# Kernel optimization log

Hardware: AMD Instinct MI355X
Metric: run time of the kernel (lower is better)

Reference implementation:

```python
import jax, jax.numpy as jnp
import numpy as np

K = 3
PAD = 1
KP = K * K


def setup_inputs() -> dict:
    key = jax.random.key(0)
    k1, k2, k3, k4 = jax.random.split(key, 4)
    B, C, O, H, W = 8, 64, 64, 128, 128
    x = jax.random.normal(k1, (B, C, H, W), dtype=jnp.float32)
    offset = jax.random.normal(k2, (B, 2 * KP, H, W), dtype=jnp.float32)
    weight = jax.random.normal(k3, (O, C, K, K), dtype=jnp.float32) * 0.05
    bias = jax.random.normal(k4, (O,), dtype=jnp.float32) * 0.05
    return {"x": x, "offset": offset, "weight": weight, "bias": bias}


def _deform_conv(x, offset, weight, bias):
    B, C, H, W = x.shape
    O = weight.shape[0]
    x_pad = jnp.pad(x, ((0, 0), (0, 0), (PAD, PAD), (PAD, PAD)))
    Hp, Wp = H + 2 * PAD, W + 2 * PAD
    dt = x.dtype

    # kernel-point grid, row-major (yy, xx) as in torch meshgrid 'ij'
    r = K // 2
    rng = jnp.arange(-r, r + 1, dtype=dt)
    ky = jnp.repeat(rng, K)          # [KP]
    kx = jnp.tile(rng, K)            # [KP]

    base_y = jnp.arange(H, dtype=dt) + PAD
    base_x = jnp.arange(W, dtype=dt) + PAD

    off = offset.reshape(B, KP, 2, H, W)
    # sample coords in padded-image space; grid_sample align_corners=True
    # normalization cancels exactly, so sample at (cy, cx) directly.
    cy = base_y[None, None, :, None] + ky[None, :, None, None] + off[:, :, 0]  # [B,KP,H,W]
    cx = base_x[None, None, None, :] + kx[None, :, None, None] + off[:, :, 1]

    y0 = jnp.floor(cy)
    x0 = jnp.floor(cx)
    wy1 = cy - y0
    wx1 = cx - x0
    wy0 = 1.0 - wy1
    wx0 = 1.0 - wx1

    flat = x_pad.reshape(B, C, Hp * Wp)

    def gather(yi, xi):
        # zeros padding: out-of-bounds corner pixels contribute 0
        valid = ((yi >= 0) & (yi <= Hp - 1) & (xi >= 0) & (xi <= Wp - 1)).astype(dt)
        yc = jnp.clip(yi, 0, Hp - 1).astype(jnp.int32)
        xc = jnp.clip(xi, 0, Wp - 1).astype(jnp.int32)
        idx = (yc * Wp + xc).reshape(B, 1, KP * H * W)
        g = jnp.take_along_axis(flat, jnp.broadcast_to(idx, (B, C, KP * H * W)), axis=2)
        g = g.reshape(B, C, KP, H, W)
        return g * valid[:, None]  # broadcast valid [B,1,KP,H,W]

    sampled = (wy0 * wx0)[:, None] * gather(y0, x0) \
            + (wy0 * wx1)[:, None] * gather(y0, x0 + 1) \
            + (wy1 * wx0)[:, None] * gather(y0 + 1, x0) \
            + (wy1 * wx1)[:, None] * gather(y0 + 1, x0 + 1)  # [B,C,KP,H,W]

    w3 = weight.reshape(O, C, KP)
    out = jnp.einsum('bcphw,ocp->bohw', sampled, w3) + bias[None, :, None, None]
    return out


def reference(x, offset, weight, bias):
    return _deform_conv(x, offset, weight, bias)
```

## Files before the change

### kernel.cpp

```cpp
#include <hip/hip_runtime.h>
#include <hip/hip_bf16.h>

#define BB 8
#define CC 64
#define OO 64
#define HH 128
#define WW 128
#define HP 130
#define WP 130
#define KP 9

typedef __attribute__((ext_vector_type(8))) _Float16 f16x8;
typedef __attribute__((ext_vector_type(2))) _Float16 h2;
typedef __attribute__((ext_vector_type(4))) float f32x4;
typedef __attribute__((ext_vector_type(4))) unsigned u32x4;

#define ROWB 16640u

static __device__ __forceinline__ unsigned short f2h(float f) {
  _Float16 h = (_Float16)f;
  return __builtin_bit_cast(unsigned short, h);
}
static __device__ __forceinline__ h2 asH2(unsigned u) {
  return __builtin_bit_cast(h2, u);
}
static __device__ __forceinline__ unsigned asU32(h2 v) {
  return __builtin_bit_cast(unsigned, v);
}

__global__ __launch_bounds__(256) void k_xpose(const float* __restrict__ x,
                                               unsigned short* __restrict__ xt) {
  __shared__ unsigned short tile[128][66];
  int wg0 = blockIdx.x;
  int wg = (wg0 & 7) * 128 + (wg0 >> 3);
  int h = wg & 127, b = wg >> 7;
  int t = threadIdx.x;
  int w = t & 127, chalf = t >> 7;
  const float* xp = x + ((size_t)(b * CC) * HH + h) * WW;
#pragma unroll 4
  for (int c2 = 0; c2 < 32; ++c2) {
    int c = c2 * 2 + chalf;
    float v = xp[(size_t)c * HH * WW + w];
    tile[w][c] = f2h(v);
  }
  __syncthreads();
  int c = t & 63, w2 = t >> 6;
  unsigned short* xtb = xt + (size_t)b * HP * WP * CC;
#pragma unroll 4
  for (int w4 = 0; w4 < 32; ++w4) {
    int ww = w4 * 4 + w2;
    xtb[((size_t)(h + 1) * WP + (ww + 1)) * CC + c] = tile[ww][c];
  }
  if (t < 128) {
    int xx = (t >= 64) ? (WP - 1) : 0;
    xtb[((size_t)(h + 1) * WP + xx) * CC + (t & 63)] = 0;
  }
  if (h == 0) {
    for (int i = t; i < 2 * WP * CC; i += 256) {
      int top = (i < WP * CC);
      int rem = top ? i : i - WP * CC;
      size_t y = top ? 0 : (HP - 1);
      xtb[y * WP * CC + rem] = 0;
    }
  }
}

__global__ __launch_bounds__(256) void k_wfrag(const float* __restrict__ wsrc,
                                               unsigned short* __restrict__ wf) {
  int flat = blockIdx.x * 256 + threadIdx.x;
  int j = flat & 7;
  int lane = (flat >> 3) & 63;
  int nf = (flat >> 9) & 3;
  int ks = (flat >> 11) & 1;
  int p = flat >> 12;
  int c = ks * 32 + ((lane >> 4) * 8) + j;
  int o = nf * 16 + (lane & 15);
  wf[flat] = f2h(wsrc[(size_t)(o * CC + c) * KP + p]);
}

__global__ __launch_bounds__(256) void k_deform_main(const float* __restrict__ offset,
                                                     const float* __restrict__ bias,
                                                     const unsigned short* __restrict__ xt,
                                                     const unsigned short* __restrict__ wf,
                                                     float* __restrict__ out) {
  __shared__ __align__(16) char lds[20992];
  int wg0 = blockIdx.x;
  int wgs = (wg0 & 7) * 256 + (wg0 >> 3);
  int tile = wgs & 1, h = (wgs >> 1) & 127, b = wgs >> 8;
  int w0 = tile * 64;
  int t = threadIdx.x, wave = t >> 6, lane = t & 63;

  char* S0 = lds;
  uint2* cw = reinterpret_cast<uint2*>(lds + 16384) + wave * 144;

#pragma unroll
  for (int it = 0; it < 3; ++it) {
    int pair = it * 64 + lane;
    if (pair < 144) {
      int p = pair >> 4, pxl = pair & 15;
      int px = wave * 16 + pxl;
      int w = w0 + px;
      const float* offp = offset + (((size_t)b * 18 + 2 * p) * HH + h) * WW + w;
      float offy = offp[0];
      float offx = offp[HH * WW];
      float cy = (float)(h + p / 3) + offy;
      float cx = (float)(w + p % 3) + offx;
      float y0f = floorf(cy), x0f = floorf(cx);
      float wy1 = cy - y0f, wx1 = cx - x0f;
      int iy0 = (int)y0f, ix0 = (int)x0f;
      int iy0c = min(max(iy0, 0), HP - 1);
      int iy1c = min(max(iy0 + 1, 0), HP - 1);
      int ix0c = min(max(ix0, 0), WP - 1);
      int ix1c = min(max(ix0 + 1, 0), WP - 1);
      unsigned w0p = (unsigned)((iy0c * WP + ix0c) * (CC * 2));
      if (ix1c != ix0c) w0p |= (1u << 30);
      if (iy1c != iy0c) w0p |= (1u << 31);
      unsigned hv;
      asm("v_cvt_pkrtz_f16_f32 %0, %1, %2" : "=v"(hv) : "v"(wy1), "v"(wx1));
      uint2 ce;
      ce.x = w0p;
      ce.y = hv;
      cw[pair] = ce;
    }
  }

  f32x4 acc[4];
#pragma unroll
  for (int m = 0; m < 4; ++m) acc[m] = (f32x4){0.f, 0.f, 0.f, 0.f};

  const char* xb = (const char*)(xt + (size_t)b * HP * WP * CC);
  int c8 = lane & 7, pg = lane >> 3;
  unsigned cb = (unsigned)c8 * 16;
  unsigned swz = cb ^ ((unsigned)pg << 4);
  const uint2* cwl = cw + pg;

#define GLOADX(dst, voff) \
  asm volatile("global_load_dwordx4 %0, %1, %2" \
               : "=v"(dst) : "v"(voff), "s"(xb) : "memory")
#define GLOADW(dst, voff) \
  asm volatile("global_load_dwordx4 %0, %1, %2" \
               : "=v"(dst) : "v"(voff), "s"(wf) : "memory")

  auto LOADC = [&](int p, uint2* eo) {
#pragma unroll
    for (int it = 0; it < 2; ++it) eo[it] = cwl[p * 16 + it * 8];
  };
  auto ISSUE = [&](const uint2* ei, u32x4* go) {
#pragma unroll
    for (int it = 0; it < 2; ++it) {
      unsigned w0p = ei[it].x;
      unsigned a00 = (w0p & 0x003FFFFFu) + cb;
      unsigned dx = ((w0p >> 30) & 1u) << 7;
      unsigned dy = (w0p & 0x80000000u) ? ROWB : 0u;
      unsigned a01 = a00 + dx, a10 = a00 + dy, a11 = a10 + dx;
      GLOADX(go[it * 4 + 0], a00);
      GLOADX(go[it * 4 + 1], a01);
      GLOADX(go[it * 4 + 2], a10);
      GLOADX(go[it * 4 + 3], a11);
    }
  };
  auto BUILD = [&](const uint2* ei, const u32x4* gi, char* Sc) {
    char* swave = Sc + wave * 2048 + pg * 128;
#pragma unroll
    for (int it = 0; it < 2; ++it) {
      h2 wyx = asH2(ei[it].y);
      _Float16 wy = wyx.x, wx = wyx.y;
      _Float16 w11 = wy * wx;
      _Float16 w01 = wx - w11;
      _Float16 w10 = wy - w11;
      _Float16 w00 = (_Float16)1.0f - wx - w10;
      h2 W00 = {w00, w00}, W01 = {w01, w01}, W10 = {w10, w10}, W11 = {w11, w11};
      u32x4 q00 = gi[it * 4 + 0], q01 = gi[it * 4 + 1];
      u32x4 q10 = gi[it * 4 + 2], q11 = gi[it * 4 + 3];
      u32x4 pk;
#pragma unroll
      for (int k = 0; k < 4; ++k) {
        h2 s = W00 * asH2(q00[k]) + W01 * asH2(q01[k])
             + W10 * asH2(q10[k]) + W11 * asH2(q11[k]);
        pk[k] = asU32(s);
      }
      *reinterpret_cast<u32x4*>(swave + it * 1024 + swz) = pk;
    }
  };
  auto MFMA = [&](const char* Sc, f16x8 b0, f16x8 b1) {
    int l15 = lane & 15, kc = (lane >> 4) * 16, sw = (lane & 7) << 4;
#pragma unroll
    for (int m = 0; m < 4; ++m) {
      int rb = (m * 16 + l15) * 128;
      f16x8 a0 = *reinterpret_cast<const f16x8*>(Sc + rb + (kc ^ sw));
      f16x8 a1 = *reinterpret_cast<const f16x8*>(Sc + rb + ((64 + kc) ^ sw));
      acc[m] = __builtin_amdgcn_mfma_f32_16x16x32_f16(a0, b0, acc[m], 0, 0, 0);
      acc[m] = __builtin_amdgcn_mfma_f32_16x16x32_f16(a1, b1, acc[m], 0, 0, 0);
    }
  };

  uint2 e[2];
  u32x4 g[8];
  LOADC(0, e);
  ISSUE(e, g);
#pragma unroll
  for (int p = 0; p < 9; ++p) {
    char* Sc = S0 + (p & 1) * 8192;
    f16x8 bv0, bv1;
    unsigned wfo = (unsigned)((p * 8 + wave) * 1024 + lane * 16);
    GLOADW(bv0, wfo);
    GLOADW(bv1, wfo + 4096);
    asm volatile("s_waitcnt vmcnt(2)" ::: "memory");
    __builtin_amdgcn_sched_barrier(0);
    BUILD(e, g, Sc);
    if (p < 8) LOADC(p + 1, e);
    asm volatile("s_waitcnt lgkmcnt(0)" ::: "memory");
    __builtin_amdgcn_s_barrier();
    if (p < 8) {
      ISSUE(e, g);
      asm volatile("s_waitcnt vmcnt(8)" ::: "memory");
    } else {
      asm volatile("s_waitcnt vmcnt(0)" ::: "memory");
    }
    __builtin_amdgcn_sched_barrier(0);
    MFMA(Sc, bv0, bv1);
  }
#undef GLOADX
#undef GLOADW

  __syncthreads();
  float* S2 = reinterpret_cast<float*>(lds);
  int l15 = lane & 15;
#pragma unroll
  for (int m = 0; m < 4; ++m) {
#pragma unroll
    for (int i2 = 0; i2 < 4; ++i2) {
      int px = m * 16 + ((lane >> 4) * 4) + i2;
      int o = wave * 16 + l15;
      S2[px * 65 + o] = acc[m][i2];
    }
  }
  __syncthreads();
  {
    int px = t & 63, o2 = t >> 6;
    float* op = out + (((size_t)b * OO) * HH + h) * WW + w0 + px;
#pragma unroll
    for (int o4 = 0; o4 < 16; ++o4) {
      int o = o4 * 4 + o2;
      op[(size_t)o * HH * WW] = S2[px * 65 + o] + bias[o];
    }
  }
}

extern "C" void kernel_launch(void* const* d_in, const int* in_sizes, int n_in,
                              void* d_out, int out_size, void* d_ws, size_t ws_size,
                              hipStream_t stream) {
  const float* x = (const float*)d_in[0];
  const float* offset = (const float*)d_in[1];
  const float* weight = (const float*)d_in[2];
  const float* bias = (const float*)d_in[3];
  float* out = (float*)d_out;

  unsigned short* xt = (unsigned short*)d_ws;
  unsigned short* wf = (unsigned short*)((char*)d_ws + 17305600);

  k_xpose<<<BB * HH, 256, 0, stream>>>(x, xt);
  k_wfrag<<<144, 256, 0, stream>>>(weight, wf);
  k_deform_main<<<BB * HH * 2, 256, 0, stream>>>(offset, bias, xt, wf, out);
}
```

Measured before the change: 48.52 us.

## Fold weight repack into transpose kernel and retile main kernel to 32-pixel blocks

The separate weight-fragment kernel is merged into the transpose kernel: its first 144 blocks also write the fp16 weight fragments, which removes one kernel launch. The main deform kernel now uses 2 waves of 128 threads covering 32 pixels per block instead of 4 waves covering 64 pixels. Each wave now computes 32 output channels using two MFMA N-fragments, and the grid is doubled. The aim is a smaller LDS footprint and more resident blocks for better latency hiding. In exchange, each wave loads more weight registers, and there are twice as many blocks, each paying its own setup and epilogue cost.

```diff
diff --git a/kernel.cpp b/kernel.cpp
--- a/kernel.cpp
+++ b/kernel.cpp
@@ -29,12 +29,25 @@
 }
 
 __global__ __launch_bounds__(256) void k_xpose(const float* __restrict__ x,
-                                               unsigned short* __restrict__ xt) {
+                                               const float* __restrict__ wsrc,
+                                               unsigned short* __restrict__ xt,
+                                               unsigned short* __restrict__ wf) {
   __shared__ unsigned short tile[128][66];
   int wg0 = blockIdx.x;
+  int t = threadIdx.x;
+  if (wg0 < 144) {
+    int flat = wg0 * 256 + t;
+    int j = flat & 7;
+    int lane = (flat >> 3) & 63;
+    int nf = (flat >> 9) & 3;
+    int ks = (flat >> 11) & 1;
+    int p = flat >> 12;
+    int c = ks * 32 + ((lane >> 4) * 8) + j;
+    int o = nf * 16 + (lane & 15);
+    wf[flat] = f2h(wsrc[(size_t)(o * CC + c) * KP + p]);
+  }
   int wg = (wg0 & 7) * 128 + (wg0 >> 3);
   int h = wg & 127, b = wg >> 7;
-  int t = threadIdx.x;
   int w = t & 127, chalf = t >> 7;
   const float* xp = x + ((size_t)(b * CC) * HH + h) * WW;
 #pragma unroll 4
@@ -65,41 +78,27 @@
   }
 }
 
-__global__ __launch_bounds__(256) void k_wfrag(const float* __restrict__ wsrc,
-                                               unsigned short* __restrict__ wf) {
-  int flat = blockIdx.x * 256 + threadIdx.x;
-  int j = flat & 7;
-  int lane = (flat >> 3) & 63;
-  int nf = (flat >> 9) & 3;
-  int ks = (flat >> 11) & 1;
-  int p = flat >> 12;
-  int c = ks * 32 + ((lane >> 4) * 8) + j;
-  int o = nf * 16 + (lane & 15);
-  wf[flat] = f2h(wsrc[(size_t)(o * CC + c) * KP + p]);
-}
-
-__global__ __launch_bounds__(256) void k_deform_main(const float* __restrict__ offset,
+__global__ __launch_bounds__(128) void k_deform_main(const float* __restrict__ offset,
                                                      const float* __restrict__ bias,
                                                      const unsigned short* __restrict__ xt,
                                                      const unsigned short* __restrict__ wf,
                                                      float* __restrict__ out) {
-  __shared__ __align__(16) char lds[20992];
+  __shared__ __align__(16) char lds[10496];
   int wg0 = blockIdx.x;
-  int wgs = (wg0 & 7) * 256 + (wg0 >> 3);
-  int tile = wgs & 1, h = (wgs >> 1) & 127, b = wgs >> 8;
-  int w0 = tile * 64;
+  int wgs = (wg0 & 7) * 512 + (wg0 >> 3);
+  int tile = wgs & 3, h = (wgs >> 2) & 127, b = wgs >> 9;
+  int w0 = tile * 32;
   int t = threadIdx.x, wave = t >> 6, lane = t & 63;
 
   char* S0 = lds;
-  uint2* cw = reinterpret_cast<uint2*>(lds + 16384) + wave * 144;
+  uint2* cw = reinterpret_cast<uint2*>(lds + 8192) + wave * 144;
 
 #pragma unroll
   for (int it = 0; it < 3; ++it) {
     int pair = it * 64 + lane;
     if (pair < 144) {
       int p = pair >> 4, pxl = pair & 15;
-      int px = wave * 16 + pxl;
-      int w = w0 + px;
+      int w = w0 + wave * 16 + pxl;
       const float* offp = offset + (((size_t)b * 18 + 2 * p) * HH + h) * WW + w;
       float offy = offp[0];
       float offx = offp[HH * WW];
@@ -182,15 +181,17 @@
       *reinterpret_cast<u32x4*>(swave + it * 1024 + swz) = pk;
     }
   };
-  auto MFMA = [&](const char* Sc, f16x8 b0, f16x8 b1) {
+  auto MFMA = [&](const char* Sc, f16x8 b00, f16x8 b01, f16x8 b10, f16x8 b11) {
     int l15 = lane & 15, kc = (lane >> 4) * 16, sw = (lane & 7) << 4;
 #pragma unroll
-    for (int m = 0; m < 4; ++m) {
+    for (int m = 0; m < 2; ++m) {
       int rb = (m * 16 + l15) * 128;
       f16x8 a0 = *reinterpret_cast<const f16x8*>(Sc + rb + (kc ^ sw));
       f16x8 a1 = *reinterpret_cast<const f16x8*>(Sc + rb + ((64 + kc) ^ sw));
-      acc[m] = __builtin_amdgcn_mfma_f32_16x16x32_f16(a0, b0, acc[m], 0, 0, 0);
-      acc[m] = __builtin_amdgcn_mfma_f32_16x16x32_f16(a1, b1, acc[m], 0, 0, 0);
+      acc[m * 2 + 0] = __builtin_amdgcn_mfma_f32_16x16x32_f16(a0, b00, acc[m * 2 + 0], 0, 0, 0);
+      acc[m * 2 + 0] = __builtin_amdgcn_mfma_f32_16x16x32_f16(a1, b01, acc[m * 2 + 0], 0, 0, 0);
+      acc[m * 2 + 1] = __builtin_amdgcn_mfma_f32_16x16x32_f16(a0, b10, acc[m * 2 + 1], 0, 0, 0);
+      acc[m * 2 + 1] = __builtin_amdgcn_mfma_f32_16x16x32_f16(a1, b11, acc[m * 2 + 1], 0, 0, 0);
     }
   };
 
@@ -200,12 +201,14 @@
   ISSUE(e, g);
 #pragma unroll
   for (int p = 0; p < 9; ++p) {
-    char* Sc = S0 + (p & 1) * 8192;
-    f16x8 bv0, bv1;
-    unsigned wfo = (unsigned)((p * 8 + wave) * 1024 + lane * 16);
-    GLOADW(bv0, wfo);
-    GLOADW(bv1, wfo + 4096);
-    asm volatile("s_waitcnt vmcnt(2)" ::: "memory");
+    char* Sc = S0 + (p & 1) * 4096;
+    f16x8 bv00, bv01, bv10, bv11;
+    unsigned wfo = (unsigned)((p * 8 + wave * 2) * 1024 + lane * 16);
+    GLOADW(bv00, wfo);
+    GLOADW(bv01, wfo + 4096);
+    GLOADW(bv10, wfo + 1024);
+    GLOADW(bv11, wfo + 5120);
+    asm volatile("s_waitcnt vmcnt(4)" ::: "memory");
     __builtin_amdgcn_sched_barrier(0);
     BUILD(e, g, Sc);
     if (p < 8) LOADC(p + 1, e);
@@ -218,7 +221,7 @@
       asm volatile("s_waitcnt vmcnt(0)" ::: "memory");
     }
     __builtin_amdgcn_sched_barrier(0);
-    MFMA(Sc, bv0, bv1);
+    MFMA(Sc, bv00, bv01, bv10, bv11);
   }
 #undef GLOADX
 #undef GLOADW
@@ -227,17 +230,20 @@
   float* S2 = reinterpret_cast<float*>(lds);
   int l15 = lane & 15;
 #pragma unroll
-  for (int m = 0; m < 4; ++m) {
-#pragma unroll
-    for (int i2 = 0; i2 < 4; ++i2) {
-      int px = m * 16 + ((lane >> 4) * 4) + i2;
-      int o = wave * 16 + l15;
-      S2[px * 65 + o] = acc[m][i2];
+  for (int m = 0; m < 2; ++m) {
+#pragma unroll
+    for (int nf = 0; nf < 2; ++nf) {
+#pragma unroll
+      for (int i2 = 0; i2 < 4; ++i2) {
+        int px = m * 16 + ((lane >> 4) * 4) + i2;
+        int o = wave * 32 + nf * 16 + l15;
+        S2[px * 65 + o] = acc[m * 2 + nf][i2];
+      }
     }
   }
   __syncthreads();
   {
-    int px = t & 63, o2 = t >> 6;
+    int px = t & 31, o2 = t >> 5;
     float* op = out + (((size_t)b * OO) * HH + h) * WW + w0 + px;
 #pragma unroll
     for (int o4 = 0; o4 < 16; ++o4) {
@@ -259,7 +265,6 @@
   unsigned short* xt = (unsigned short*)d_ws;
   unsigned short* wf = (unsigned short*)((char*)d_ws + 17305600);
 
-  k_xpose<<<BB * HH, 256, 0, stream>>>(x, xt);
-  k_wfrag<<<144, 256, 0, stream>>>(weight, wf);
-  k_deform_main<<<BB * HH * 2, 256, 0, stream>>>(offset, bias, xt, wf, out);
-}
+  k_xpose<<<BB * HH, 256, 0, stream>>>(x, weight, xt, wf);
+  k_deform_main<<<BB * HH * 4, 128, 0, stream>>>(offset, bias, xt, wf, out);
+}
```

Measured after the change: 50.27 us. 3.6% more time.
